# Kernel tuning notes

Measured on AMD Instinct MI355X. Metric: run time of the kernel, lower is better.

## Reference

```python
import jax, jax.numpy as jnp
import numpy as np

B, F, L, P = 64, 512, 512, 96
HT, HF = 8, 8  # temporal / feature attention heads
EPS_ATTN = 1e-6
EPS_LN = 1e-5
EPS_REVIN = 1e-5


def _layernorm(x, g, b):
    m = x.mean(axis=-1, keepdims=True)
    v = x.var(axis=-1, keepdims=True)
    return (x - m) / jnp.sqrt(v + EPS_LN) * g + b


def _lin_attn(x, Wq, bq, Wk, bk, Wv, bv, Wo, bo, H):
    # x: (B, N, D). Katharopoulos linear attention with elu+1 feature map.
    Bz, N, D = x.shape
    hd = D // H

    def proj(W, b):
        return (x @ W.T + b).reshape(Bz, N, H, hd).transpose(0, 2, 1, 3)  # (B,H,N,hd)

    Q = jax.nn.elu(proj(Wq, bq)) + 1.0
    K = jax.nn.elu(proj(Wk, bk)) + 1.0
    V = proj(Wv, bv)
    KV = jnp.einsum('bhnd,bhne->bhde', K, V)           # (B,H,hd,hd)
    out = jnp.einsum('bhnd,bhde->bhne', Q, KV)         # (B,H,N,hd)
    Z = K.sum(axis=2)                                  # (B,H,hd)
    norm = jnp.einsum('bhnd,bhd->bhn', Q, Z)[..., None] + EPS_ATTN
    out = (out / norm).transpose(0, 2, 1, 3).reshape(Bz, N, D)
    return out @ Wo.T + bo


def setup_inputs() -> dict:
    key = jax.random.key(0)
    ks = jax.random.split(key, 32)
    s = 0.1  # xavier-ish gain

    def w(k, shape, fan):
        return jax.random.normal(k, shape, dtype=jnp.float32) * (s / np.sqrt(fan))

    inp = {
        'x': jax.random.normal(ks[0], (B, F, L), dtype=jnp.float32),
        # RevIN affine
        'rg': jnp.ones((1, 1, F), jnp.float32),
        'rb': jnp.zeros((1, 1, F), jnp.float32),
        # LayerNorms
        'n1g': jnp.ones((F,), jnp.float32), 'n1b': jnp.zeros((F,), jnp.float32),
        'n2g': jnp.ones((L,), jnp.float32), 'n2b': jnp.zeros((L,), jnp.float32),
        # temporal attention (dim=F)
        'tWq': w(ks[1], (F, F), F), 'tbq': jnp.zeros((F,), jnp.float32),
        'tWk': w(ks[2], (F, F), F), 'tbk': jnp.zeros((F,), jnp.float32),
        'tWv': w(ks[3], (F, F), F), 'tbv': jnp.zeros((F,), jnp.float32),
        'tWo': w(ks[4], (F, F), F), 'tbo': jnp.zeros((F,), jnp.float32),
        # feature attention (dim=L)
        'fWq': w(ks[5], (L, L), L), 'fbq': jnp.zeros((L,), jnp.float32),
        'fWk': w(ks[6], (L, L), L), 'fbk': jnp.zeros((L,), jnp.float32),
        'fWv': w(ks[7], (L, L), L), 'fbv': jnp.zeros((L,), jnp.float32),
        'fWo': w(ks[8], (L, L), L), 'fbo': jnp.zeros((L,), jnp.float32),
        # individual per-feature Linear bank: seq_len -> pred_len
        'Wlin': w(ks[9], (F, P, L), L), 'blin': jnp.zeros((F, P), jnp.float32),
        # projector F -> 1
        'Wproj': w(ks[10], (1, F), F), 'bproj': jnp.zeros((1,), jnp.float32),
    }
    return inp


def reference(x, rg, rb, n1g, n1b,
              tWq, tbq, tWk, tbk, tWv, tbv, tWo, tbo,
              n2g, n2b,
              fWq, fbq, fWk, fbk, fWv, fbv, fWo, fbo,
              Wlin, blin, Wproj, bproj):
    # (B, F, L) -> (B, L, F)
    h = x.transpose(0, 2, 1)
    # RevIN norm (stats detached, std is unbiased like torch.std)
    mean = jax.lax.stop_gradient(h.mean(axis=1, keepdims=True))
    std = jax.lax.stop_gradient(jnp.std(h, axis=1, keepdims=True, ddof=1) + EPS_REVIN)
    h = (h - mean) / std * rg + rb

    # Dual linear attention
    r = h
    h = _layernorm(h, n1g, n1b)
    h = _lin_attn(h, tWq, tbq, tWk, tbk, tWv, tbv, tWo, tbo, HT) + r
    h = h.transpose(0, 2, 1)  # (B, F, L)
    r = h
    h = _layernorm(h, n2g, n2b)
    h = _lin_attn(h, fWq, fbq, fWk, fbk, fWv, fbv, fWo, fbo, HF) + r
    # (module transposes back to (B,L,F) then LinearCrypto permutes to (B,F,L);
    #  we stay in (B,F,L))

    # individual per-feature linear: seq_len -> pred_len
    y = jnp.einsum('bfl,fpl->bfp', h, Wlin) + blin[None]  # (B,F,P)
    y = y.transpose(0, 2, 1)                              # (B,P,F)
    # RevIN denorm
    y = (y - rb) / rg
    y = y * std + mean
    # projector F -> 1
    out = y @ Wproj.T + bproj  # (B,P,1)
    return out[..., 0]
```

## Files before the change

kernel.cpp:

```cpp
#include <hip/hip_runtime.h>
#include <hip/hip_bf16.h>
#include <cstdint>
#include <cstddef>


#define EPS_ATTN 1e-6f
#define EPS_LN   1e-5f
#define EPS_REVIN 1e-5f

typedef __attribute__((ext_vector_type(8))) short bf16x8;
typedef __attribute__((ext_vector_type(4))) float f32x4;
typedef __attribute__((ext_vector_type(8))) unsigned short u16x8;

__device__ __forceinline__ float bf2f(unsigned short u) {
  unsigned int x = ((unsigned int)u) << 16;
  return __builtin_bit_cast(float, x);
}
__device__ __forceinline__ unsigned short f2bf(float f) {
  __hip_bfloat16 h = __float2bfloat16(f);
  return __builtin_bit_cast(unsigned short, h);
}
__device__ __forceinline__ void gload16(const void* g, void* l) {
  __builtin_amdgcn_global_load_lds(
      (const __attribute__((address_space(1))) void*)g,
      (__attribute__((address_space(3))) void*)l, 16, 0, 0);
}

__global__ __launch_bounds__(256) void revin_xn_k(const float* __restrict__ x,
                                                  const float* __restrict__ rg,
                                                  const float* __restrict__ rb,
                                                  float* __restrict__ meanb,
                                                  float* __restrict__ stdb,
                                                  unsigned short* __restrict__ xn) {
  int wid = threadIdx.x >> 6, lane = threadIdx.x & 63;
  int row = blockIdx.x * 4 + wid;
  const float* xr = x + (size_t)row * 512 + lane * 8;
  float4 a = *(const float4*)xr;
  float4 c = *(const float4*)(xr + 4);
  float s1 = a.x + a.y + a.z + a.w + c.x + c.y + c.z + c.w;
  float s2 = a.x * a.x + a.y * a.y + a.z * a.z + a.w * a.w +
             c.x * c.x + c.y * c.y + c.z * c.z + c.w * c.w;
#pragma unroll
  for (int off = 1; off < 64; off <<= 1) { s1 += __shfl_xor(s1, off); s2 += __shfl_xor(s2, off); }
  float m = s1 * (1.f / 512.f);
  float var = fmaxf((s2 - 512.f * m * m) * (1.f / 511.f), 0.f);
  float sd = sqrtf(var) + EPS_REVIN;
  int f = row & 511;
  float sc = rg[f] / sd;
  float of = rb[f] - m * sc;
  u16x8 o;
  o[0] = f2bf(a.x * sc + of); o[1] = f2bf(a.y * sc + of);
  o[2] = f2bf(a.z * sc + of); o[3] = f2bf(a.w * sc + of);
  o[4] = f2bf(c.x * sc + of); o[5] = f2bf(c.y * sc + of);
  o[6] = f2bf(c.z * sc + of); o[7] = f2bf(c.w * sc + of);
  *(u16x8*)(xn + (size_t)row * 512 + lane * 8) = o;
  if (lane == 0) { meanb[row] = m; stdb[row] = sd; }
}

__global__ __launch_bounds__(256) void tln_k(const unsigned short* __restrict__ xn,
                                             const float* __restrict__ g,
                                             const float* __restrict__ bq,
                                             unsigned short* __restrict__ o16) {
  __shared__ unsigned short Ts[32][528] __attribute__((aligned(16)));
  const int b = blockIdx.y, l0 = blockIdx.x * 32;
  const int tid = threadIdx.x;
#pragma unroll
  for (int it = 0; it < 8; ++it) {
    int idx = it * 256 + tid;
    int f = idx >> 2, lc = (idx & 3) * 8;
    u16x8 v = *(const u16x8*)(xn + ((size_t)b * 512 + f) * 512 + l0 + lc);
#pragma unroll
    for (int j = 0; j < 8; ++j) Ts[lc + j][f] = v[j];
  }
  __syncthreads();
  const int l = tid >> 3, q = tid & 7;
  float s1 = 0.f, s2 = 0.f;
#pragma unroll
  for (int i = 0; i < 8; ++i) {
    int c = (i + q) & 7;
    bf16x8 t = *(const bf16x8*)&Ts[l][q * 64 + c * 8];
#pragma unroll
    for (int j = 0; j < 8; ++j) {
      float x = bf2f((unsigned short)t[j]);
      s1 += x; s2 += x * x;
    }
  }
#pragma unroll
  for (int off = 1; off < 8; off <<= 1) { s1 += __shfl_xor(s1, off); s2 += __shfl_xor(s2, off); }
  float m = s1 * (1.f / 512.f);
  float var = fmaxf(s2 * (1.f / 512.f) - m * m, 0.f);
  float iv = 1.f / sqrtf(var + EPS_LN);
#pragma unroll
  for (int i = 0; i < 8; ++i) {
    int c = (i + q) & 7;
    int f8 = q * 64 + c * 8;
    bf16x8 t = *(const bf16x8*)&Ts[l][f8];
    float4 g0 = *(const float4*)(g + f8);
    float4 g1 = *(const float4*)(g + f8 + 4);
    float4 b0 = *(const float4*)(bq + f8);
    float4 b1 = *(const float4*)(bq + f8 + 4);
    u16x8 o;
    o[0] = f2bf((bf2f((unsigned short)t[0]) - m) * iv * g0.x + b0.x);
    o[1] = f2bf((bf2f((unsigned short)t[1]) - m) * iv * g0.y + b0.y);
    o[2] = f2bf((bf2f((unsigned short)t[2]) - m) * iv * g0.z + b0.z);
    o[3] = f2bf((bf2f((unsigned short)t[3]) - m) * iv * g0.w + b0.w);
    o[4] = f2bf((bf2f((unsigned short)t[4]) - m) * iv * g1.x + b1.x);
    o[5] = f2bf((bf2f((unsigned short)t[5]) - m) * iv * g1.y + b1.y);
    o[6] = f2bf((bf2f((unsigned short)t[6]) - m) * iv * g1.z + b1.z);
    o[7] = f2bf((bf2f((unsigned short)t[7]) - m) * iv * g1.w + b1.w);
    *(u16x8*)&Ts[l][f8] = o;
  }
  __syncthreads();
#pragma unroll
  for (int it = 0; it < 8; ++it) {
    int idx = it * 256 + tid;
    int ll = idx >> 6, f8 = (idx & 63) * 8;
    u16x8 v = *(const u16x8*)&Ts[ll][f8];
    *(u16x8*)(o16 + ((size_t)b * 512 + l0 + ll) * 512 + f8) = v;
  }
}

__global__ __launch_bounds__(256) void ln_k(const unsigned short* __restrict__ in,
                                            const float* __restrict__ g,
                                            const float* __restrict__ bq,
                                            unsigned short* __restrict__ o16) {
  int row = blockIdx.x * 4 + (threadIdx.x >> 6);
  int lane = threadIdx.x & 63;
  u16x8 u = *(const u16x8*)(in + (size_t)row * 512 + lane * 8);
  float v[8];
#pragma unroll
  for (int j = 0; j < 8; ++j) v[j] = bf2f(u[j]);
  float s1 = 0.f, s2 = 0.f;
#pragma unroll
  for (int j = 0; j < 8; ++j) { s1 += v[j]; s2 += v[j] * v[j]; }
#pragma unroll
  for (int off = 1; off < 64; off <<= 1) { s1 += __shfl_xor(s1, off); s2 += __shfl_xor(s2, off); }
  float m = s1 * (1.f / 512.f);
  float var = fmaxf(s2 * (1.f / 512.f) - m * m, 0.f);
  float iv = 1.f / sqrtf(var + EPS_LN);
  float4 g0 = *(const float4*)(g + lane * 8);
  float4 g1 = *(const float4*)(g + lane * 8 + 4);
  float4 b0 = *(const float4*)(bq + lane * 8);
  float4 b1 = *(const float4*)(bq + lane * 8 + 4);
  u16x8 o;
  o[0] = f2bf((v[0] - m) * iv * g0.x + b0.x);
  o[1] = f2bf((v[1] - m) * iv * g0.y + b0.y);
  o[2] = f2bf((v[2] - m) * iv * g0.z + b0.z);
  o[3] = f2bf((v[3] - m) * iv * g0.w + b0.w);
  o[4] = f2bf((v[4] - m) * iv * g1.x + b1.x);
  o[5] = f2bf((v[5] - m) * iv * g1.y + b1.y);
  o[6] = f2bf((v[6] - m) * iv * g1.z + b1.z);
  o[7] = f2bf((v[7] - m) * iv * g1.w + b1.w);
  *(u16x8*)(o16 + (size_t)row * 512 + lane * 8) = o;
}

__global__ __launch_bounds__(256) void wconv_k(const float* w0, const float* w1,
                                               const float* w2, const float* w3,
                                               const float* w4, const float* w5,
                                               const float* w6, const float* w7,
                                               unsigned short* __restrict__ out) {
  const float* srcs[8] = {w0, w1, w2, w3, w4, w5, w6, w7};
  const float* s = srcs[blockIdx.y];
  size_t idx = (size_t)blockIdx.x * 2048 + threadIdx.x * 8;
  float4 v0 = *(const float4*)(s + idx);
  float4 v1 = *(const float4*)(s + idx + 4);
  u16x8 o;
  o[0] = f2bf(v0.x); o[1] = f2bf(v0.y); o[2] = f2bf(v0.z); o[3] = f2bf(v0.w);
  o[4] = f2bf(v1.x); o[5] = f2bf(v1.y); o[6] = f2bf(v1.z); o[7] = f2bf(v1.w);
  *(u16x8*)(out + (size_t)blockIdx.y * 262144 + idx) = o;
}

__device__ __forceinline__ void gemm_core(const unsigned short* __restrict__ A,
                                          const unsigned short* __restrict__ W,
                                          unsigned short* smem,
                                          f32x4 (&acc)[4][4],
                                          int m0, int wrow, int tid, int koff) {
  const int w = tid >> 6, lane = tid & 63;
  const int wr = w >> 1, wc = w & 1;
  const int r8 = lane >> 3, s8 = lane & 7, gslot = s8 ^ r8;
  const unsigned short* Ag = A + (size_t)(m0 + w * 32 + r8) * 512 + gslot * 8;
  const unsigned short* Wg = W + (size_t)(wrow + w * 32 + r8) * 512 + gslot * 8;
  unsigned short* Asw = smem + w * 2048;
  unsigned short* Bsw = smem + 8192 + w * 2048;
  for (int kk = 0; kk < 8; ++kk) {
    const int k0 = ((kk + koff) & 7) * 64;
#pragma unroll
    for (int c = 0; c < 4; ++c) {
      gload16(Ag + (size_t)c * 8 * 512 + k0, Asw + c * 512);
      gload16(Wg + (size_t)c * 8 * 512 + k0, Bsw + c * 512);
    }
    __syncthreads();
#pragma unroll
    for (int s = 0; s < 2; ++s) {
      bf16x8 fa[4], fb[4];
#pragma unroll
      for (int i = 0; i < 4; ++i) {
        int ra = wr * 64 + i * 16 + (lane & 15);
        int sa = (s * 4 + (lane >> 4)) ^ (ra & 7);
        fa[i] = *(const bf16x8*)&smem[ra * 64 + sa * 8];
        int rb = wc * 64 + i * 16 + (lane & 15);
        int sb = (s * 4 + (lane >> 4)) ^ (rb & 7);
        fb[i] = *(const bf16x8*)&smem[8192 + rb * 64 + sb * 8];
      }
#pragma unroll
      for (int i = 0; i < 4; ++i)
#pragma unroll
        for (int j = 0; j < 4; ++j)
          acc[i][j] = __builtin_amdgcn_mfma_f32_16x16x32_bf16(fa[i], fb[j], acc[i][j], 0, 0, 0);
    }
    __syncthreads();
  }
}

template <int TRANS, int ACT, int RES>
__device__ __forceinline__ void gemm_epilogue(f32x4 (&acc)[4][4],
                                              unsigned short* Cs,
                                              const float* __restrict__ bias,
                                              const unsigned short* __restrict__ resid,
                                              unsigned short* __restrict__ out,
                                              int m0, int n0, int tid) {
  const int w = tid >> 6, lane = tid & 63;
  const int wr = w >> 1, wc = w & 1;
  const int ro = (lane >> 4) * 4, c16 = lane & 15;
#pragma unroll
  for (int j = 0; j < 4; ++j) {
    int nl = wc * 64 + j * 16 + c16;
    float bi = bias[n0 + nl];
#pragma unroll
    for (int i = 0; i < 4; ++i) {
      int ml = wr * 64 + i * 16 + ro;
#pragma unroll
      for (int r = 0; r < 4; ++r) {
        float v = acc[i][j][r] + bi;
        if constexpr (ACT) v = (v > 0.f) ? v + 1.f : __expf(v);
        if constexpr (TRANS) Cs[nl * 136 + ml + r] = f2bf(v);
        else                 Cs[(ml + r) * 136 + nl] = f2bf(v);
      }
    }
  }
  __syncthreads();
  size_t rowbase; int colbase;
  if constexpr (TRANS) { rowbase = (size_t)((m0 >> 9) * 512 + n0); colbase = m0 & 511; }
  else                 { rowbase = (size_t)m0; colbase = n0; }
#pragma unroll
  for (int c = 0; c < 8; ++c) {
    int idx = c * 256 + tid;
    int rr = idx >> 4, c8 = (idx & 15) * 8;
    u16x8 v = *(const u16x8*)&Cs[rr * 136 + c8];
    size_t gaddr = (rowbase + rr) * 512 + colbase + c8;
    if constexpr (RES) {
      u16x8 rv = *(const u16x8*)(resid + gaddr);
#pragma unroll
      for (int q = 0; q < 8; ++q) v[q] = f2bf(bf2f(v[q]) + bf2f(rv[q]));
    }
    *(u16x8*)(out + gaddr) = v;
  }
}

template <int TRANS, int ACT, int RES>
__global__ __launch_bounds__(256, 4) void gemm_std_k(const unsigned short* __restrict__ A,
                                                     const unsigned short* __restrict__ W,
                                                     const float* __restrict__ bias,
                                                     const unsigned short* __restrict__ resid,
                                                     unsigned short* __restrict__ out) {
  __shared__ unsigned short smem[17408] __attribute__((aligned(16)));
  const int tid = threadIdx.x;
  const int bid = blockIdx.x;
  const int nb = (bid & 7) * 128 + (bid >> 3);
  const int m0 = (nb >> 2) * 128;
  const int n0 = (nb & 3) * 128;
  f32x4 acc[4][4] = {};
  gemm_core(A, W, smem, acc, m0, n0, tid, (bid >> 3) & 7);
  gemm_epilogue<TRANS, ACT, RES>(acc, smem, bias, resid, out, m0, n0, tid);
}

__global__ __launch_bounds__(256, 4) void gemm_qkv3_k(const unsigned short* __restrict__ A,
                                                      const unsigned short* __restrict__ Wqkv,
                                                      const float* __restrict__ bq,
                                                      const float* __restrict__ bk,
                                                      const float* __restrict__ bv,
                                                      unsigned short* __restrict__ Q,
                                                      unsigned short* __restrict__ K,
                                                      unsigned short* __restrict__ V) {
  __shared__ unsigned short smem[17408] __attribute__((aligned(16)));
  const int tid = threadIdx.x;
  const unsigned int bid = blockIdx.x;
  const unsigned int nb = (bid & 7) * 384 + (bid >> 3);
  const int mi = nb / 12, ni = nb % 12;
  const int m0 = mi * 128;
  const int mat = ni >> 2;
  const int n0 = (ni & 3) * 128;
  f32x4 acc[4][4] = {};
  gemm_core(A, Wqkv, smem, acc, m0, mat * 512 + n0, tid, (bid >> 3) & 7);

  const float* bias = (mat == 0) ? bq : (mat == 1) ? bk : bv;
  unsigned short* out = (mat == 0) ? Q : (mat == 1) ? K : V;
  const bool trans = (mat > 0);
  const bool act = (mat < 2);

  const int w = tid >> 6, lane = tid & 63;
  const int wr = w >> 1, wc = w & 1;
  const int ro = (lane >> 4) * 4, c16 = lane & 15;
  unsigned short* Cs = smem;
#pragma unroll
  for (int j = 0; j < 4; ++j) {
    int nl = wc * 64 + j * 16 + c16;
    float bi = bias[n0 + nl];
#pragma unroll
    for (int i = 0; i < 4; ++i) {
      int ml = wr * 64 + i * 16 + ro;
#pragma unroll
      for (int r = 0; r < 4; ++r) {
        float v = acc[i][j][r] + bi;
        if (act) v = (v > 0.f) ? v + 1.f : __expf(v);
        int row = trans ? nl : (ml + r);
        int col = trans ? (ml + r) : nl;
        Cs[row * 136 + col] = f2bf(v);
      }
    }
  }
  __syncthreads();
  size_t rowbase = trans ? (size_t)((m0 >> 9) * 512 + n0) : (size_t)m0;
  int colbase = trans ? (m0 & 511) : n0;
#pragma unroll
  for (int c = 0; c < 8; ++c) {
    int idx = c * 256 + tid;
    int rr = idx >> 4, c8 = (idx & 15) * 8;
    u16x8 v = *(const u16x8*)&Cs[rr * 136 + c8];
    *(u16x8*)(out + (rowbase + rr) * 512 + colbase + c8) = v;
  }
}

__global__ __launch_bounds__(256) void kv_mfma_k(const unsigned short* __restrict__ KT,
                                                 const unsigned short* __restrict__ VT,
                                                 unsigned short* __restrict__ KVTo,
                                                 float* __restrict__ Zo) {
  int bh = blockIdx.x;
  int tid = threadIdx.x, w = tid >> 6, lane = tid & 63;
  int r16 = lane & 15, g = lane >> 4;
  const unsigned short* vb = VT + ((size_t)bh * 64 + w * 16 + r16) * 512 + g * 8;
  const unsigned short* kb = KT + ((size_t)bh * 64 + r16) * 512 + g * 8;
  const short ob = (short)0x3F80;
  const bf16x8 onesf = {ob, ob, ob, ob, ob, ob, ob, ob};
  f32x4 acc[4] = {};
  f32x4 zacc[4] = {};
  for (int n0 = 0; n0 < 512; n0 += 32) {
    bf16x8 vf = *(const bf16x8*)(vb + n0);
#pragma unroll
    for (int j = 0; j < 4; ++j) {
      bf16x8 kf = *(const bf16x8*)(kb + (size_t)j * 16 * 512 + n0);
      acc[j] = __builtin_amdgcn_mfma_f32_16x16x32_bf16(vf, kf, acc[j], 0, 0, 0);
      zacc[j] = __builtin_amdgcn_mfma_f32_16x16x32_bf16(onesf, kf, zacc[j], 0, 0, 0);
    }
  }
  int e = w * 16 + g * 4;
  unsigned short* kvo = KVTo + (size_t)bh * 4096;
#pragma unroll
  for (int j = 0; j < 4; ++j)
#pragma unroll
    for (int r = 0; r < 4; ++r)
      kvo[(size_t)(e + r) * 64 + j * 16 + r16] = f2bf(acc[j][r]);
  if (w == 0 && g == 0) {
#pragma unroll
    for (int j = 0; j < 4; ++j) Zo[(size_t)bh * 64 + j * 16 + r16] = zacc[j][0];
  }
}

__global__ __launch_bounds__(512) void attn_mfma_k(unsigned short* __restrict__ Q16,
                                                   const unsigned short* __restrict__ KVT,
                                                   const float* __restrict__ Z) {
  __shared__ unsigned short kvs[32768] __attribute__((aligned(16)));
  __shared__ float Zs[512];
  int tid = threadIdx.x;
  int b = blockIdx.x >> 2;
  int m0 = blockIdx.x * 128;
  const unsigned short* kg = KVT + (size_t)b * 32768;
#pragma unroll
  for (int t = 0; t < 8; ++t) {
    int c = tid + t * 512;
    int e = (c >> 3) & 63;
    u16x8 v = *(const u16x8*)(kg + (size_t)c * 8);
    *(u16x8*)((char*)kvs + ((c * 16) ^ ((e & 7) << 4))) = v;
  }
  Zs[tid] = Z[(size_t)b * 512 + tid];
  __syncthreads();

  int w = tid >> 6, lane = tid & 63;
  int r16 = lane & 15, g = lane >> 4;
  unsigned short* qrow = Q16 + (size_t)(m0 + w * 16 + r16) * 512;
  int orow0 = m0 + w * 16 + g * 4;

  for (int h = 0; h < 8; ++h) {
    bf16x8 q0 = *(const bf16x8*)(qrow + h * 64 + g * 8);
    bf16x8 q1 = *(const bf16x8*)(qrow + h * 64 + 32 + g * 8);
    const float* zh = Zs + h * 64;
    float np = 0.f;
#pragma unroll
    for (int q = 0; q < 8; ++q) np = fmaf(bf2f((unsigned short)q0[q]), zh[g * 8 + q], np);
#pragma unroll
    for (int q = 0; q < 8; ++q) np = fmaf(bf2f((unsigned short)q1[q]), zh[32 + g * 8 + q], np);

    f32x4 acc[4] = {};
#pragma unroll
    for (int j = 0; j < 4; ++j) {
      int e = j * 16 + r16;
      int byte0 = h * 8192 + e * 128;
      int sw = (e & 7) << 4;
      bf16x8 k0 = *(const bf16x8*)((char*)kvs + ((byte0 + g * 16) ^ sw));
      bf16x8 k1 = *(const bf16x8*)((char*)kvs + ((byte0 + 64 + g * 16) ^ sw));
      acc[j] = __builtin_amdgcn_mfma_f32_16x16x32_bf16(q0, k0, acc[j], 0, 0, 0);
      acc[j] = __builtin_amdgcn_mfma_f32_16x16x32_bf16(q1, k1, acc[j], 0, 0, 0);
    }
    np += __shfl_xor(np, 16);
    np += __shfl_xor(np, 32);
    float inv = 1.f / (np + EPS_ATTN);
    float inv4[4];
#pragma unroll
    for (int r = 0; r < 4; ++r) inv4[r] = __shfl(inv, g * 4 + r);
#pragma unroll
    for (int j = 0; j < 4; ++j)
#pragma unroll
      for (int r = 0; r < 4; ++r)
        Q16[(size_t)(orow0 + r) * 512 + h * 64 + j * 16 + r16] = f2bf(acc[j][r] * inv4[r]);
  }
}

__global__ __launch_bounds__(256) void feat_linear_k(const unsigned short* __restrict__ h3,
                                                     const float* __restrict__ Wlin,
                                                     const float* __restrict__ blin,
                                                     float* __restrict__ Y) {
  __shared__ unsigned short As[64 * 64] __attribute__((aligned(16)));
  __shared__ unsigned short Bs[96 * 64] __attribute__((aligned(16)));
  const int f = blockIdx.x;
  const int tid = threadIdx.x;
  const int w = tid >> 6, lane = tid & 63;
  const int r16 = lane & 15, g = lane >> 4;
  const int r8 = lane >> 3, s8 = lane & 7, gs = s8 ^ r8;

  f32x4 acc[6] = {};
  for (int k0 = 0; k0 < 512; k0 += 64) {
#pragma unroll
    for (int c = 0; c < 2; ++c) {
      int row = w * 16 + c * 8 + r8;
      gload16(h3 + ((size_t)row * 512 + f) * 512 + k0 + gs * 8,
              As + (w * 16 + c * 8) * 64);
    }
#pragma unroll
    for (int it = 0; it < 3; ++it) {
      int idx = it * 256 + tid;
      int pp = idx >> 3, sl = idx & 7;
      const float* src = Wlin + ((size_t)f * 96 + pp) * 512 + k0 + sl * 8;
      float4 v0 = *(const float4*)src;
      float4 v1 = *(const float4*)(src + 4);
      u16x8 o;
      o[0] = f2bf(v0.x); o[1] = f2bf(v0.y); o[2] = f2bf(v0.z); o[3] = f2bf(v0.w);
      o[4] = f2bf(v1.x); o[5] = f2bf(v1.y); o[6] = f2bf(v1.z); o[7] = f2bf(v1.w);
      *(u16x8*)&Bs[pp * 64 + (sl ^ (pp & 7)) * 8] = o;
    }
    __syncthreads();
#pragma unroll
    for (int s = 0; s < 2; ++s) {
      int arow = w * 16 + r16;
      bf16x8 fa = *(const bf16x8*)&As[arow * 64 + (((s * 4 + g) ^ (arow & 7)) * 8)];
#pragma unroll
      for (int n = 0; n < 6; ++n) {
        int brow = n * 16 + r16;
        bf16x8 fb = *(const bf16x8*)&Bs[brow * 64 + (((s * 4 + g) ^ (brow & 7)) * 8)];
        acc[n] = __builtin_amdgcn_mfma_f32_16x16x32_bf16(fa, fb, acc[n], 0, 0, 0);
      }
    }
    __syncthreads();
  }
  const int b0 = w * 16 + g * 4;
#pragma unroll
  for (int n = 0; n < 6; ++n) {
    float bi = blin[f * 96 + n * 16 + r16];
#pragma unroll
    for (int r = 0; r < 4; ++r)
      Y[((size_t)(b0 + r) * 512 + f) * 96 + n * 16 + r16] = acc[n][r] + bi;
  }
}

__global__ __launch_bounds__(256) void final_out_k(const float* __restrict__ Y,
                                                   const float* __restrict__ meanb,
                                                   const float* __restrict__ stdb,
                                                   const float* __restrict__ rg,
                                                   const float* __restrict__ rb,
                                                   const float* __restrict__ Wproj,
                                                   const float* __restrict__ bproj,
                                                   float* __restrict__ out) {
  int b = blockIdx.x;
  __shared__ float cs[512];
  __shared__ float kred[4];
  int t = threadIdx.x;
  float kpart = 0.f;
  for (int f = t; f < 512; f += 256) {
    float sd = stdb[b * 512 + f], mn = meanb[b * 512 + f];
    float g = rg[f], rbv = rb[f], wp = Wproj[f];
    float c = wp * sd / g;
    cs[f] = c;
    kpart += wp * mn - c * rbv;
  }
#pragma unroll
  for (int off = 32; off; off >>= 1) kpart += __shfl_down(kpart, off);
  int wid = t >> 6, lane = t & 63;
  if (lane == 0) kred[wid] = kpart;
  __syncthreads();
  float K = kred[0] + kred[1] + kred[2] + kred[3] + bproj[0];
  if (t < 96) {
    float acc = 0.f;
    for (int f = 0; f < 512; ++f) acc = fmaf(cs[f], Y[((size_t)b * 512 + f) * 96 + t], acc);
    out[b * 96 + t] = acc + K;
  }
}

extern "C" void kernel_launch(void* const* d_in, const int* in_sizes, int n_in,
                              void* d_out, int out_size, void* d_ws, size_t ws_size,
                              hipStream_t stream) {
  const float* x    = (const float*)d_in[0];
  const float* rg   = (const float*)d_in[1];
  const float* rb   = (const float*)d_in[2];
  const float* n1g  = (const float*)d_in[3];
  const float* n1b  = (const float*)d_in[4];
  const float* n2g  = (const float*)d_in[5];
  const float* n2b  = (const float*)d_in[6];
  const float* tWq  = (const float*)d_in[7];
  const float* tbq  = (const float*)d_in[8];
  const float* tWk  = (const float*)d_in[9];
  const float* tbk  = (const float*)d_in[10];
  const float* tWv  = (const float*)d_in[11];
  const float* tbv  = (const float*)d_in[12];
  const float* tWo  = (const float*)d_in[13];
  const float* tbo  = (const float*)d_in[14];
  const float* fWq  = (const float*)d_in[15];
  const float* fbq  = (const float*)d_in[16];
  const float* fWk  = (const float*)d_in[17];
  const float* fbk  = (const float*)d_in[18];
  const float* fWv  = (const float*)d_in[19];
  const float* fbv  = (const float*)d_in[20];
  const float* fWo  = (const float*)d_in[21];
  const float* fbo  = (const float*)d_in[22];
  const float* Wlin = (const float*)d_in[23];
  const float* blin = (const float*)d_in[24];
  const float* Wprj = (const float*)d_in[25];
  const float* bprj = (const float*)d_in[26];
  float* out = (float*)d_out;

  const size_t SZ = (size_t)64 * 512 * 512;
  char* p = (char*)d_ws;
  unsigned short* xn  = (unsigned short*)p; p += SZ * 2;
  unsigned short* h2  = (unsigned short*)p; p += SZ * 2;
  unsigned short* h3  = (unsigned short*)p; p += SZ * 2;
  unsigned short* abf = (unsigned short*)p; p += SZ * 2;
  unsigned short* q16 = (unsigned short*)p; p += SZ * 2;
  unsigned short* k16 = (unsigned short*)p; p += SZ * 2;
  unsigned short* v16 = (unsigned short*)p; p += SZ * 2;
  unsigned short* wbf = (unsigned short*)p; p += (size_t)8 * 262144 * 2;
  unsigned short* kvt = (unsigned short*)p; p += (size_t)512 * 4096 * 2;
  float* z     = (float*)p;         p += (size_t)512 * 64 * 4;
  float* meanb = (float*)p;         p += 32768 * 4;
  float* stdb  = (float*)p;         p += 32768 * 4;
  float* ybuf  = (float*)abf;

  wconv_k<<<dim3(128, 8), 256, 0, stream>>>(tWq, tWk, tWv, tWo, fWq, fWk, fWv, fWo, wbf);
  revin_xn_k<<<8192, 256, 0, stream>>>(x, rg, rb, meanb, stdb, xn);

  tln_k<<<dim3(16, 64), 256, 0, stream>>>(xn, n1g, n1b, abf);
  gemm_qkv3_k<<<3072, 256, 0, stream>>>(abf, wbf, tbq, tbk, tbv, q16, k16, v16);
  kv_mfma_k<<<512, 256, 0, stream>>>(k16, v16, kvt, z);
  attn_mfma_k<<<256, 512, 0, stream>>>(q16, kvt, z);
  gemm_std_k<1, 0, 1><<<1024, 256, 0, stream>>>(q16, wbf + 3 * 262144, tbo, xn, h2);

  ln_k<<<8192, 256, 0, stream>>>(h2, n2g, n2b, abf);
  gemm_qkv3_k<<<3072, 256, 0, stream>>>(abf, wbf + 4 * 262144, fbq, fbk, fbv, q16, k16, v16);
  kv_mfma_k<<<512, 256, 0, stream>>>(k16, v16, kvt, z);
  attn_mfma_k<<<256, 512, 0, stream>>>(q16, kvt, z);
  gemm_std_k<0, 0, 1><<<1024, 256, 0, stream>>>(q16, wbf + 7 * 262144, fbo, h2, h3);

  feat_linear_k<<<512, 256, 0, stream>>>(h3, Wlin, blin, ybuf);
  final_out_k<<<64, 256, 0, stream>>>(ybuf, meanb, stdb, rg, rb, Wprj, bprj, out);
}
```

Baseline: 381.4 us.

## Load GEMM MFMA fragments directly from global memory, bypassing LDS staging

Replaces the LDS-staged GEMM mainloop, which copied tiles with global_load_lds, synchronised and read swizzled fragments, with direct per-lane 16-byte global loads into MFMA operand registers. This removes the LDS round trip and the two barriers per k-step. The cost is that each A and W element is now fetched by both waves that share it, and loads are strided 1 KB rows, so more traffic lands on L1/L2. The occupancy hint of 4 in launch_bounds is dropped and the k-offset staggering is removed.

```diff
diff --git a/kernel.cpp b/kernel.cpp
--- a/kernel.cpp
+++ b/kernel.cpp
@@ -170,45 +170,29 @@
   *(u16x8*)(out + (size_t)blockIdx.y * 262144 + idx) = o;
 }
 
-__device__ __forceinline__ void gemm_core(const unsigned short* __restrict__ A,
-                                          const unsigned short* __restrict__ W,
-                                          unsigned short* smem,
-                                          f32x4 (&acc)[4][4],
-                                          int m0, int wrow, int tid, int koff) {
+__device__ __forceinline__ void gemm_core_reg(const unsigned short* __restrict__ A,
+                                              const unsigned short* __restrict__ W,
+                                              f32x4 (&acc)[4][4],
+                                              int m0, int wrow, int tid) {
   const int w = tid >> 6, lane = tid & 63;
   const int wr = w >> 1, wc = w & 1;
-  const int r8 = lane >> 3, s8 = lane & 7, gslot = s8 ^ r8;
-  const unsigned short* Ag = A + (size_t)(m0 + w * 32 + r8) * 512 + gslot * 8;
-  const unsigned short* Wg = W + (size_t)(wrow + w * 32 + r8) * 512 + gslot * 8;
-  unsigned short* Asw = smem + w * 2048;
-  unsigned short* Bsw = smem + 8192 + w * 2048;
-  for (int kk = 0; kk < 8; ++kk) {
-    const int k0 = ((kk + koff) & 7) * 64;
-#pragma unroll
-    for (int c = 0; c < 4; ++c) {
-      gload16(Ag + (size_t)c * 8 * 512 + k0, Asw + c * 512);
-      gload16(Wg + (size_t)c * 8 * 512 + k0, Bsw + c * 512);
-    }
-    __syncthreads();
-#pragma unroll
-    for (int s = 0; s < 2; ++s) {
-      bf16x8 fa[4], fb[4];
-#pragma unroll
-      for (int i = 0; i < 4; ++i) {
-        int ra = wr * 64 + i * 16 + (lane & 15);
-        int sa = (s * 4 + (lane >> 4)) ^ (ra & 7);
-        fa[i] = *(const bf16x8*)&smem[ra * 64 + sa * 8];
-        int rb = wc * 64 + i * 16 + (lane & 15);
-        int sb = (s * 4 + (lane >> 4)) ^ (rb & 7);
-        fb[i] = *(const bf16x8*)&smem[8192 + rb * 64 + sb * 8];
-      }
-#pragma unroll
-      for (int i = 0; i < 4; ++i)
-#pragma unroll
-        for (int j = 0; j < 4; ++j)
-          acc[i][j] = __builtin_amdgcn_mfma_f32_16x16x32_bf16(fa[i], fb[j], acc[i][j], 0, 0, 0);
-    }
-    __syncthreads();
+  const int r16 = lane & 15, ks = lane >> 4;
+  const unsigned short* Ab = A + (size_t)(m0 + wr * 64 + r16) * 512 + ks * 8;
+  const unsigned short* Wb = W + (size_t)(wrow + wc * 64 + r16) * 512 + ks * 8;
+#pragma unroll 4
+  for (int kc = 0; kc < 16; ++kc) {
+    bf16x8 fa[4], fb[4];
+#pragma unroll
+    for (int i = 0; i < 4; ++i)
+      fa[i] = *(const bf16x8*)(Ab + (size_t)i * 16 * 512 + kc * 32);
+#pragma unroll
+    for (int j = 0; j < 4; ++j)
+      fb[j] = *(const bf16x8*)(Wb + (size_t)j * 16 * 512 + kc * 32);
+#pragma unroll
+    for (int i = 0; i < 4; ++i)
+#pragma unroll
+      for (int j = 0; j < 4; ++j)
+        acc[i][j] = __builtin_amdgcn_mfma_f32_16x16x32_bf16(fa[i], fb[j], acc[i][j], 0, 0, 0);
   }
 }
 
@@ -258,11 +242,11 @@
 }
 
 template <int TRANS, int ACT, int RES>
-__global__ __launch_bounds__(256, 4) void gemm_std_k(const unsigned short* __restrict__ A,
-                                                     const unsigned short* __restrict__ W,
-                                                     const float* __restrict__ bias,
-                                                     const unsigned short* __restrict__ resid,
-                                                     unsigned short* __restrict__ out) {
+__global__ __launch_bounds__(256) void gemm_std_k(const unsigned short* __restrict__ A,
+                                                  const unsigned short* __restrict__ W,
+                                                  const float* __restrict__ bias,
+                                                  const unsigned short* __restrict__ resid,
+                                                  unsigned short* __restrict__ out) {
   __shared__ unsigned short smem[17408] __attribute__((aligned(16)));
   const int tid = threadIdx.x;
   const int bid = blockIdx.x;
@@ -270,18 +254,18 @@
   const int m0 = (nb >> 2) * 128;
   const int n0 = (nb & 3) * 128;
   f32x4 acc[4][4] = {};
-  gemm_core(A, W, smem, acc, m0, n0, tid, (bid >> 3) & 7);
+  gemm_core_reg(A, W, acc, m0, n0, tid);
   gemm_epilogue<TRANS, ACT, RES>(acc, smem, bias, resid, out, m0, n0, tid);
 }
 
-__global__ __launch_bounds__(256, 4) void gemm_qkv3_k(const unsigned short* __restrict__ A,
-                                                      const unsigned short* __restrict__ Wqkv,
-                                                      const float* __restrict__ bq,
-                                                      const float* __restrict__ bk,
-                                                      const float* __restrict__ bv,
-                                                      unsigned short* __restrict__ Q,
-                                                      unsigned short* __restrict__ K,
-                                                      unsigned short* __restrict__ V) {
+__global__ __launch_bounds__(256) void gemm_qkv3_k(const unsigned short* __restrict__ A,
+                                                   const unsigned short* __restrict__ Wqkv,
+                                                   const float* __restrict__ bq,
+                                                   const float* __restrict__ bk,
+                                                   const float* __restrict__ bv,
+                                                   unsigned short* __restrict__ Q,
+                                                   unsigned short* __restrict__ K,
+                                                   unsigned short* __restrict__ V) {
   __shared__ unsigned short smem[17408] __attribute__((aligned(16)));
   const int tid = threadIdx.x;
   const unsigned int bid = blockIdx.x;
@@ -291,7 +275,7 @@
   const int mat = ni >> 2;
   const int n0 = (ni & 3) * 128;
   f32x4 acc[4][4] = {};
-  gemm_core(A, Wqkv, smem, acc, m0, mat * 512 + n0, tid, (bid >> 3) & 7);
+  gemm_core_reg(A, Wqkv, acc, m0, mat * 512 + n0, tid);
 
   const float* bias = (mat == 0) ? bq : (mat == 1) ? bk : bv;
   unsigned short* out = (mat == 0) ? Q : (mat == 1) ? K : V;
```

Result: slower. 722.9 us (+89.5%).
